# Kernel tuning notes

Measured on AMD Instinct MI355X. Metric: run time of the kernel, lower is better.

## Reference

```python
import jax, jax.numpy as jnp
import numpy as np

P = 16        # patch size
SIM = 0.3     # similarity threshold (forward default arg `sim`)
STY_STD = 1000.0


def patchify(imgs):
    # (N,3,H,W) -> (N, h*w, p*p*3)
    N, C, H, W = imgs.shape
    h, w = H // P, W // P
    x = imgs.reshape(N, C, h, P, w, P)
    x = jnp.einsum('nchpwq->nhwpqc', x)
    return x.reshape(N, h * w, P * P * C)


def setup_inputs() -> dict:
    key = jax.random.key(0)
    k1, k2, k3, k4 = jax.random.split(key, 4)
    N, L, D = 2, 196, 768
    x = jax.random.normal(k1, (N, L + 1, D), dtype=jnp.float32)
    imgs = jax.random.normal(k2, (N, 3, 224, 224), dtype=jnp.float32)
    # torch trunc_normal_(std=1000, a=-2, b=2) == truncated normal on [-2,2]
    learnable_sty = (jax.random.truncated_normal(
        k3, -2.0 / STY_STD, 2.0 / STY_STD, (N, L, L, 1), dtype=jnp.float32) * STY_STD)
    noise = jax.random.normal(k4, (N, L, L, 1), dtype=jnp.float32)
    return {"x": x, "imgs": imgs, "learnable_sty": learnable_sty, "noise": noise}


def reference(x, imgs, learnable_sty, noise):
    imgs = patchify(imgs)                                   # (N, L, 768)
    cls_tokens, x = x[:, :1], x[:, 1:]
    N, L, D = x.shape

    # per-patch normalization (torch.var default is unbiased -> ddof=1)
    mean = imgs.mean(axis=-1, keepdims=True)
    var = jnp.var(imgs, axis=-1, keepdims=True, ddof=1)
    imgs_n = (imgs - mean) / jnp.sqrt(var + 1e-6)
    nrm = jnp.linalg.norm(imgs_n, axis=-1)                  # (N, L)
    Sim = jnp.einsum('aik,ajk->aij', imgs_n, imgs_n) / (nrm[:, :, None] * nrm[:, None, :])

    M0 = jnp.triu((Sim > SIM).astype(jnp.float32))          # (N, L, L), binary
    rows = jnp.arange(L)

    def body(i, M):
        # original loop breaks when sum == N*L; we freeze M once that holds
        done = M.sum() == N * L
        mask = (M[:, i, :] == 0).astype(M.dtype)            # (N, L)
        # rows <= i unchanged (M*M == M for binary), rows > i masked
        upd = jnp.where(rows[None, :, None] > i, M * mask[:, None, :], M)
        return jnp.where(done, M, upd)

    M = jax.lax.fori_loop(0, L - 1, body, M0)

    # decompose: phase (con) keeps grad, amplitude (sty) is detached
    fft = jnp.fft.fftn(x, axes=(-1,))
    con, sty = jnp.angle(fft), jnp.abs(fft)
    sty_d = jax.lax.stop_gradient(sty)

    avg_sum = (M[..., None] * sty_d[:, None, :, :]).sum(axis=2)   # (N, L, D)
    sty_mask = (avg_sum > 0).astype(jnp.float32)                   # (N, L, D)
    num = M.sum(axis=2)[..., None]                                 # (N, L, 1)
    avg = avg_sum / jnp.clip(num, 1e-7, None)                      # (N, L, D)
    std = jnp.sqrt(
        (M[..., None] * (sty_d[:, None, :, :] - avg[:, :, None, :]) ** 2).sum(axis=2)
        / jnp.clip(num, 1e-7, None))                               # (N, L, D)

    sty_para = sty_mask[:, None, :, :] * learnable_sty             # (N, L, L, D)
    sty_para = sty_para / jnp.clip(sty_para.sum(axis=2, keepdims=True), 1e-7, None)
    various = noise * std[:, None, :, :] + avg[:, None, :, :]      # (N, L, L, D)
    sum_sty = (sty_para * various).sum(axis=2)                     # (N, L, D)

    # compose: ifft(amp * e^{i phase}), torch .float() keeps the real part
    out = jnp.real(jnp.fft.ifftn(sum_sty * jnp.exp(1j * con), axes=(-1,))).astype(jnp.float32)
    return jnp.concatenate((cls_tokens, out), axis=1)
```

## Files before the change

kernel.cpp:

```cpp
#include <hip/hip_runtime.h>
#include <math.h>

typedef unsigned long long u64;

#define NBATCH 2
#define LTOK 196
#define DDIM 768
#define NROWS (NBATCH*LTOK)
#define NLD (NBATCH*LTOK*DDIM)

#define PI_F 3.14159265358979323846f
#define S3 0.86602540378443864676f

__device__ __forceinline__ void fft_butterfly(float* re, float* im,
                                              const float2* T,
                                              int tau, int s, int half) {
  int sub = tau >> 7;
  int b = tau & 127;
  int j = b & (half - 1);
  int p0 = (sub << 8) + ((b >> (s - 1)) << s) + j;
  int p1 = p0 + half;
  float2 w = T[j << (8 - s)];
  float xr = re[p1], xi = im[p1];
  float tr = w.x * xr - w.y * xi;
  float ti = w.x * xi + w.y * xr;
  float ur = re[p0], ui = im[p0];
  re[p0] = ur + tr; im[p0] = ui + ti;
  re[p1] = ur - tr; im[p1] = ui - ti;
}

__device__ __forceinline__ void fft_stages(float* re, float* im,
                                           const float2* T, int t) {
#pragma unroll
  for (int s = 1; s <= 8; s++) {
    int half = 1 << (s - 1);
    fft_butterfly(re, im, T, t, s, half);
    if (t < 128) fft_butterfly(re, im, T, t + 256, s, half);
    __syncthreads();
  }
}

__global__ __launch_bounds__(256) void k_pre(const float* __restrict__ imgs,
                                             const float* __restrict__ x,
                                             float* __restrict__ uT,
                                             float* __restrict__ sty,
                                             float* __restrict__ phre,
                                             float* __restrict__ phim) {
  int t = threadIdx.x;
  if (blockIdx.x < NROWS) {
    int blk = blockIdx.x;
    int a = blk / LTOK, l = blk - a * LTOK;
    int hh = l / 14, ww = l - hh * 14;
    float loc[3];
    double s = 0.0, sq = 0.0;
#pragma unroll
    for (int e = 0; e < 3; e++) {
      int d = t + (e << 8);
      int p = d / 48, r = d - p * 48;
      int q2 = r / 3, c = r - q2 * 3;
      float val = imgs[((size_t)(a * 3 + c) * 224 + (hh * 16 + p)) * 224 + (ww * 16 + q2)];
      loc[e] = val;
      s += (double)val;
      sq += (double)val * (double)val;
    }
#pragma unroll
    for (int o = 32; o > 0; o >>= 1) { s += __shfl_down(s, o); sq += __shfl_down(sq, o); }
    __shared__ double rs[4], rq[4];
    __shared__ float sh_mu, sh_sc;
    if ((t & 63) == 0) { rs[t >> 6] = s; rq[t >> 6] = sq; }
    __syncthreads();
    if (t == 0) {
      double S = rs[0] + rs[1] + rs[2] + rs[3];
      double Q = rq[0] + rq[1] + rq[2] + rq[3];
      double mean = S / 768.0;
      double ss = Q - S * S / 768.0;
      if (ss < 1e-30) ss = 1e-30;
      sh_mu = (float)mean;
      sh_sc = (float)(1.0 / sqrt(ss));
    }
    __syncthreads();
    float mu = sh_mu, sc = sh_sc;
    int col = a * LTOK + l;
#pragma unroll
    for (int e = 0; e < 3; e++) {
      int d = t + (e << 8);
      uT[(size_t)d * NROWS + col] = (loc[e] - mu) * sc;
    }
  } else {
    int blk = blockIdx.x - NROWS;
    int a = blk / LTOK, i = blk - a * LTOK;
    __shared__ float re[768], im[768];
    __shared__ float2 t256[128];
    if (t < 128) {
      float sn, cs;
      __sincosf(-2.0f * PI_F * (float)t / 256.0f, &sn, &cs);
      t256[t] = make_float2(cs, sn);
    }
    size_t row = ((size_t)a * (LTOK + 1) + 1 + i) * DDIM;
#pragma unroll
    for (int e = 0; e < 3; e++) {
      int d = t + (e << 8);
      int m = d / 3, r = d - 3 * m;
      int p = (r << 8) + (__brev((unsigned)m) >> 24);
      re[p] = x[row + d];
      im[p] = 0.f;
    }
    __syncthreads();
    fft_stages(re, im, t256, t);
    float a0r = re[t],       a0i = im[t];
    float a1r = re[256 + t], a1i = im[256 + t];
    float a2r = re[512 + t], a2i = im[512 + t];
    float sn, cs;
    __sincosf(-2.0f * PI_F * (float)t / 768.0f, &sn, &cs);
    float2 w1 = make_float2(cs, sn);
    float2 w2 = make_float2(cs * cs - sn * sn, 2.f * cs * sn);
    float b1r = a1r * w1.x - a1i * w1.y, b1i = a1r * w1.y + a1i * w1.x;
    float b2r = a2r * w2.x - a2i * w2.y, b2i = a2r * w2.y + a2i * w2.x;
    float Xr[3], Xi[3];
    Xr[0] = a0r + b1r + b2r;
    Xi[0] = a0i + b1i + b2i;
    Xr[1] = a0r + (-0.5f * b1r + S3 * b1i) + (-0.5f * b2r - S3 * b2i);
    Xi[1] = a0i + (-0.5f * b1i - S3 * b1r) + (-0.5f * b2i + S3 * b2r);
    Xr[2] = a0r + (-0.5f * b1r - S3 * b1i) + (-0.5f * b2r + S3 * b2i);
    Xi[2] = a0i + (-0.5f * b1i + S3 * b1r) + (-0.5f * b2i - S3 * b2r);
    size_t ob = ((size_t)a * LTOK + i) * DDIM + t;
#pragma unroll
    for (int s = 0; s < 3; s++) {
      float mag = sqrtf(Xr[s] * Xr[s] + Xi[s] * Xi[s]);
      size_t o = ob + (s << 8);
      sty[o] = mag;
      if (mag > 0.f) { phre[o] = Xr[s] / mag; phim[o] = Xi[s] / mag; }
      else           { phre[o] = 1.f;         phim[o] = 0.f;         }
    }
  }
}

__global__ __launch_bounds__(256) void k_sim(const float* __restrict__ uT,
                                             u64* __restrict__ Mb) {
  int blk = blockIdx.x;
  int a = blk / LTOK, i = blk - a * LTOK;
  __shared__ float ui[768];
  __shared__ u64 mask[4];
  int t = threadIdx.x;
  if (t < 4) mask[t] = 0ull;
  int coli = a * LTOK + i;
#pragma unroll
  for (int e = 0; e < 3; e++) {
    int d = t + (e << 8);
    ui[d] = uT[(size_t)d * NROWS + coli];
  }
  __syncthreads();
  int j = i + t;
  if (j < LTOK) {
    const float* col = uT + (a * LTOK + j);
    float dot = 0.f;
#pragma unroll 8
    for (int d = 0; d < 768; d++) dot += ui[d] * col[(size_t)d * NROWS];
    if (dot > 0.3f) atomicOr(&mask[j >> 6], 1ull << (j & 63));
  }
  __syncthreads();
  if (t < 4) Mb[((size_t)a * LTOK + i) * 4 + t] = mask[t];
}

__global__ __launch_bounds__(256) void k_greedy(u64* __restrict__ Mb) {
  __shared__ u64 Ml[NROWS * 4];
  __shared__ int red[4];
  __shared__ int Sdone;
  int t = threadIdx.x;
  for (int w = t; w < NROWS * 4; w += 256) Ml[w] = Mb[w];
  __syncthreads();
  for (int i = 0; i < LTOK - 1; i++) {
    int s = 0;
    for (int w = t; w < NROWS * 4; w += 256) s += __popcll(Ml[w]);
#pragma unroll
    for (int o = 32; o > 0; o >>= 1) s += __shfl_down(s, o);
    if ((t & 63) == 0) red[t >> 6] = s;
    __syncthreads();
    if (t == 0) Sdone = ((red[0] + red[1] + red[2] + red[3]) == NROWS) ? 1 : 0;
    __syncthreads();
    if (Sdone) break;
    for (int w = t; w < NROWS * 4; w += 256) {
      int a = w / (LTOK * 4);
      int rem = w - a * (LTOK * 4);
      int r = rem >> 2, wi = rem & 3;
      if (r > i) Ml[w] &= ~Ml[(a * LTOK + i) * 4 + wi];
    }
    __syncthreads();
  }
  for (int w = t; w < NROWS * 4; w += 256) Mb[w] = Ml[w];
}

__global__ __launch_bounds__(256) void k_stats(const u64* __restrict__ Mb,
                                               const float* __restrict__ sty,
                                               float* __restrict__ savg,
                                               float* __restrict__ sstd,
                                               float* __restrict__ smsk) {
  int blk = blockIdx.x;
  int a = blk / LTOK, i = blk - a * LTOK;
  __shared__ u64 mrow[4];
  int t = threadIdx.x;
  if (t < 4) mrow[t] = Mb[((size_t)a * LTOK + i) * 4 + t];
  __syncthreads();
  int num = __popcll(mrow[0]) + __popcll(mrow[1]) + __popcll(mrow[2]) + __popcll(mrow[3]);
  float fnum = fmaxf((float)num, 1e-7f);
  float acc0 = 0.f, acc1 = 0.f, acc2 = 0.f;
  for (int w = 0; w < 4; w++) {
    u64 m = mrow[w];
    while (m) {
      int b = __ffsll(m) - 1; m &= (m - 1);
      int j = (w << 6) + b;
      const float* sr = sty + ((size_t)a * LTOK + j) * DDIM;
      acc0 += sr[t]; acc1 += sr[t + 256]; acc2 += sr[t + 512];
    }
  }
  float av0 = acc0 / fnum, av1 = acc1 / fnum, av2 = acc2 / fnum;
  float sq0 = 0.f, sq1 = 0.f, sq2 = 0.f;
  for (int w = 0; w < 4; w++) {
    u64 m = mrow[w];
    while (m) {
      int b = __ffsll(m) - 1; m &= (m - 1);
      int j = (w << 6) + b;
      const float* sr = sty + ((size_t)a * LTOK + j) * DDIM;
      float d0 = sr[t] - av0, d1 = sr[t + 256] - av1, d2 = sr[t + 512] - av2;
      sq0 += d0 * d0; sq1 += d1 * d1; sq2 += d2 * d2;
    }
  }
  size_t o = ((size_t)a * LTOK + i) * DDIM + t;
  float mk0 = acc0 > 0.f ? 1.f : 0.f;
  float mk1 = acc1 > 0.f ? 1.f : 0.f;
  float mk2 = acc2 > 0.f ? 1.f : 0.f;
  smsk[o] = mk0;            smsk[o + 256] = mk1;            smsk[o + 512] = mk2;
  savg[o] = mk0 * av0;      savg[o + 256] = mk1 * av1;      savg[o + 512] = mk2 * av2;
  sstd[o] = mk0 * sqrtf(sq0 / fnum);
  sstd[o + 256] = mk1 * sqrtf(sq1 / fnum);
  sstd[o + 512] = mk2 * sqrtf(sq2 / fnum);
}

#define RTILE 7
#define JCH 4
#define JLEN 49
__global__ __launch_bounds__(256) void k_combine_part(const float* __restrict__ ls,
                                                      const float* __restrict__ nz,
                                                      const float* __restrict__ savg,
                                                      const float* __restrict__ sstd,
                                                      const float* __restrict__ smsk,
                                                      float* __restrict__ numP,
                                                      float* __restrict__ denP) {
  int blk = blockIdx.x;
  int a = blk / 336;
  int rem = blk - a * 336;
  int it = rem / 12;
  int r2 = rem - it * 12;
  int dc = r2 >> 2;
  int jc = r2 & 3;
  int i0 = it * RTILE;
  int j0 = jc * JLEN;
  int t = threadIdx.x;
  int d = (dc << 8) + t;
  __shared__ float lsr[RTILE][JLEN], lnr[RTILE][JLEN];
  for (int idx = t; idx < RTILE * JLEN; idx += 256) {
    int ii = idx / JLEN, j = idx - ii * JLEN;
    size_t o = ((size_t)(a * LTOK + i0 + ii)) * LTOK + j0 + j;
    float l = ls[o];
    lsr[ii][j] = l;
    lnr[ii][j] = l * nz[o];
  }
  __syncthreads();
  float nm[RTILE], dn[RTILE];
#pragma unroll
  for (int ii = 0; ii < RTILE; ii++) { nm[ii] = 0.f; dn[ii] = 0.f; }
#pragma unroll 7
  for (int j = 0; j < JLEN; j++) {
    size_t b = ((size_t)(a * LTOK + j0 + j)) * DDIM + d;
    float sd = sstd[b], sv = savg[b], sm = smsk[b];
#pragma unroll
    for (int ii = 0; ii < RTILE; ii++) {
      nm[ii] += lnr[ii][j] * sd;
      nm[ii] += lsr[ii][j] * sv;
      dn[ii] += lsr[ii][j] * sm;
    }
  }
#pragma unroll
  for (int ii = 0; ii < RTILE; ii++) {
    size_t o = ((size_t)jc * NROWS + (a * LTOK + i0 + ii)) * DDIM + d;
    numP[o] = nm[ii];
    denP[o] = dn[ii];
  }
}

__global__ __launch_bounds__(256) void k_ifft(const float* __restrict__ x,
                                              const float* __restrict__ numP,
                                              const float* __restrict__ denP,
                                              const float* __restrict__ phre,
                                              const float* __restrict__ phim,
                                              float* __restrict__ out) {
  int blk = blockIdx.x;
  int t = threadIdx.x;
  if (blk < NBATCH) {
    size_t b = (size_t)blk * (LTOK + 1) * DDIM;
    out[b + t] = x[b + t];
    out[b + t + 256] = x[b + t + 256];
    out[b + t + 512] = x[b + t + 512];
    return;
  }
  int rr = blk - NBATCH;
  int a = rr / LTOK, i = rr - a * LTOK;
  __shared__ float re[768], im[768];
  __shared__ float2 t256[128];
  if (t < 128) {
    float sn, cs;
    __sincosf(2.0f * PI_F * (float)t / 256.0f, &sn, &cs);
    t256[t] = make_float2(cs, sn);
  }
  size_t rowz = ((size_t)a * LTOK + i) * DDIM;
#pragma unroll
  for (int e = 0; e < 3; e++) {
    int d = t + (e << 8);
    float num = 0.f, den = 0.f;
#pragma unroll
    for (int jc = 0; jc < JCH; jc++) {
      size_t o = (size_t)jc * NROWS * DDIM + rowz + d;
      num += numP[o];
      den += denP[o];
    }
    float mg = num / fmaxf(den, 1e-7f);
    int m = d / 3, r = d - 3 * m;
    int p = (r << 8) + (__brev((unsigned)m) >> 24);
    re[p] = mg * phre[rowz + d];
    im[p] = mg * phim[rowz + d];
  }
  __syncthreads();
  fft_stages(re, im, t256, t);
  float a0r = re[t],       a0i = im[t];
  float a1r = re[256 + t], a1i = im[256 + t];
  float a2r = re[512 + t], a2i = im[512 + t];
  float sn, cs;
  __sincosf(2.0f * PI_F * (float)t / 768.0f, &sn, &cs);
  float2 w1 = make_float2(cs, sn);
  float2 w2 = make_float2(cs * cs - sn * sn, 2.f * cs * sn);
  float b1r = a1r * w1.x - a1i * w1.y, b1i = a1r * w1.y + a1i * w1.x;
  float b2r = a2r * w2.x - a2i * w2.y, b2i = a2r * w2.y + a2i * w2.x;
  float Xr[3];
  Xr[0] = a0r + b1r + b2r;
  Xr[1] = a0r + (-0.5f * b1r - S3 * b1i) + (-0.5f * b2r + S3 * b2i);
  Xr[2] = a0r + (-0.5f * b1r + S3 * b1i) + (-0.5f * b2r - S3 * b2i);
  size_t ob = ((size_t)a * (LTOK + 1) + 1 + i) * DDIM + t;
  const float inv = 1.0f / 768.0f;
  out[ob]       = Xr[0] * inv;
  out[ob + 256] = Xr[1] * inv;
  out[ob + 512] = Xr[2] * inv;
}

extern "C" void kernel_launch(void* const* d_in, const int* in_sizes, int n_in,
                              void* d_out, int out_size, void* d_ws, size_t ws_size,
                              hipStream_t stream) {
  (void)in_sizes; (void)n_in; (void)out_size; (void)ws_size;
  const float* x    = (const float*)d_in[0];
  const float* imgs = (const float*)d_in[1];
  const float* ls   = (const float*)d_in[2];
  const float* nz   = (const float*)d_in[3];
  float* out = (float*)d_out;

  float* wf   = (float*)d_ws;
  float* uT   = wf;
  float* sty  = wf + (size_t)NLD;
  float* phre = wf + 2 * (size_t)NLD;
  float* phim = wf + 3 * (size_t)NLD;
  float* sstd = wf + 4 * (size_t)NLD;
  float* smsk = wf + 5 * (size_t)NLD;
  float* numP = wf + 6 * (size_t)NLD;
  float* denP = wf + 10 * (size_t)NLD;
  u64* Mb = (u64*)(wf + 14 * (size_t)NLD);

  k_pre         <<<2 * NROWS, 256, 0, stream>>>(imgs, x, uT, sty, phre, phim);
  k_sim         <<<NROWS, 256, 0, stream>>>(uT, Mb);
  k_greedy      <<<1, 256, 0, stream>>>(Mb);
  k_stats       <<<NROWS, 256, 0, stream>>>(Mb, sty, uT , sstd, smsk);
  k_combine_part<<<NBATCH * 28 * 3 * JCH, 256, 0, stream>>>(ls, nz, uT , sstd, smsk, numP, denP);
  k_ifft        <<<NBATCH + NROWS, 256, 0, stream>>>(x, numP, denP, phre, phim, out);
}
```

Measured before the change: 125.4 us.

## Fuse sim, FFT and greedy into one kernel; recompute stats inside combine

Restructures the pipeline from six launches to four. The FFT now runs alongside the similarity blocks, and a last-block-done atomic counter runs the greedy suppression pass inside that same kernel, so the separate single-block launch goes away. Per-row avg/std/mask are no longer stored; the combine kernel recomputes them from the mask bits and sty for each j. This drops the stats kernel and its intermediate buffers but repeats the gather work once per i-tile (28x) and relies on cross-block memory fences for correctness.

```diff
diff --git a/kernel.cpp b/kernel.cpp
--- a/kernel.cpp
+++ b/kernel.cpp
@@ -11,6 +11,10 @@
 
 #define PI_F 3.14159265358979323846f
 #define S3 0.86602540378443864676f
+
+#define RT 7
+#define JCH 4
+#define JLEN 49
 
 __device__ __forceinline__ void fft_butterfly(float* re, float* im,
                                               const float2* T,
@@ -40,61 +44,75 @@
   }
 }
 
-__global__ __launch_bounds__(256) void k_pre(const float* __restrict__ imgs,
-                                             const float* __restrict__ x,
-                                             float* __restrict__ uT,
-                                             float* __restrict__ sty,
-                                             float* __restrict__ phre,
-                                             float* __restrict__ phim) {
+__global__ __launch_bounds__(256) void k_patch(const float* __restrict__ imgs,
+                                               float* __restrict__ uT,
+                                               unsigned int* __restrict__ counter) {
+  int blk = blockIdx.x;
+  int a = blk / LTOK, l = blk - a * LTOK;
+  int hh = l / 14, ww = l - hh * 14;
   int t = threadIdx.x;
-  if (blockIdx.x < NROWS) {
-    int blk = blockIdx.x;
-    int a = blk / LTOK, l = blk - a * LTOK;
-    int hh = l / 14, ww = l - hh * 14;
-    float loc[3];
-    double s = 0.0, sq = 0.0;
-#pragma unroll
-    for (int e = 0; e < 3; e++) {
-      int d = t + (e << 8);
-      int p = d / 48, r = d - p * 48;
-      int q2 = r / 3, c = r - q2 * 3;
-      float val = imgs[((size_t)(a * 3 + c) * 224 + (hh * 16 + p)) * 224 + (ww * 16 + q2)];
-      loc[e] = val;
-      s += (double)val;
-      sq += (double)val * (double)val;
-    }
-#pragma unroll
-    for (int o = 32; o > 0; o >>= 1) { s += __shfl_down(s, o); sq += __shfl_down(sq, o); }
-    __shared__ double rs[4], rq[4];
-    __shared__ float sh_mu, sh_sc;
-    if ((t & 63) == 0) { rs[t >> 6] = s; rq[t >> 6] = sq; }
-    __syncthreads();
-    if (t == 0) {
-      double S = rs[0] + rs[1] + rs[2] + rs[3];
-      double Q = rq[0] + rq[1] + rq[2] + rq[3];
-      double mean = S / 768.0;
-      double ss = Q - S * S / 768.0;
-      if (ss < 1e-30) ss = 1e-30;
-      sh_mu = (float)mean;
-      sh_sc = (float)(1.0 / sqrt(ss));
-    }
-    __syncthreads();
-    float mu = sh_mu, sc = sh_sc;
-    int col = a * LTOK + l;
-#pragma unroll
-    for (int e = 0; e < 3; e++) {
-      int d = t + (e << 8);
-      uT[(size_t)d * NROWS + col] = (loc[e] - mu) * sc;
-    }
-  } else {
+  if (blk == 0 && t == 0) *counter = 0u;
+  float loc[3];
+  double s = 0.0, sq = 0.0;
+#pragma unroll
+  for (int e = 0; e < 3; e++) {
+    int d = t + (e << 8);
+    int p = d / 48, r = d - p * 48;
+    int q2 = r / 3, c = r - q2 * 3;
+    float val = imgs[((size_t)(a * 3 + c) * 224 + (hh * 16 + p)) * 224 + (ww * 16 + q2)];
+    loc[e] = val;
+    s += (double)val;
+    sq += (double)val * (double)val;
+  }
+#pragma unroll
+  for (int o = 32; o > 0; o >>= 1) { s += __shfl_down(s, o); sq += __shfl_down(sq, o); }
+  __shared__ double rs[4], rq[4];
+  __shared__ float sh_mu, sh_sc;
+  if ((t & 63) == 0) { rs[t >> 6] = s; rq[t >> 6] = sq; }
+  __syncthreads();
+  if (t == 0) {
+    double S = rs[0] + rs[1] + rs[2] + rs[3];
+    double Q = rq[0] + rq[1] + rq[2] + rq[3];
+    double mean = S / 768.0;
+    double ss = Q - S * S / 768.0;
+    if (ss < 1e-30) ss = 1e-30;
+    sh_mu = (float)mean;
+    sh_sc = (float)(1.0 / sqrt(ss));
+  }
+  __syncthreads();
+  float mu = sh_mu, sc = sh_sc;
+  int col = a * LTOK + l;
+#pragma unroll
+  for (int e = 0; e < 3; e++) {
+    int d = t + (e << 8);
+    uT[(size_t)d * NROWS + col] = (loc[e] - mu) * sc;
+  }
+}
+
+union SimSMem {
+  struct { float ui[768]; u64 mask[4]; } sim;
+  struct { u64 Ml[NROWS * 4]; int red[4]; int done; } greedy;
+  struct { float re[768]; float im[768]; float2 t256[128]; } fft;
+};
+
+__global__ __launch_bounds__(256) void k_simfft(const float* __restrict__ uT,
+                                                const float* __restrict__ x,
+                                                float* __restrict__ sty,
+                                                float* __restrict__ phre,
+                                                float* __restrict__ phim,
+                                                u64* __restrict__ Mb,
+                                                unsigned int* __restrict__ counter) {
+  __shared__ SimSMem sm;
+  __shared__ int s_last;
+  int t = threadIdx.x;
+
+  if (blockIdx.x >= NROWS) {
     int blk = blockIdx.x - NROWS;
     int a = blk / LTOK, i = blk - a * LTOK;
-    __shared__ float re[768], im[768];
-    __shared__ float2 t256[128];
     if (t < 128) {
       float sn, cs;
       __sincosf(-2.0f * PI_F * (float)t / 256.0f, &sn, &cs);
-      t256[t] = make_float2(cs, sn);
+      sm.fft.t256[t] = make_float2(cs, sn);
     }
     size_t row = ((size_t)a * (LTOK + 1) + 1 + i) * DDIM;
 #pragma unroll
@@ -102,14 +120,14 @@
       int d = t + (e << 8);
       int m = d / 3, r = d - 3 * m;
       int p = (r << 8) + (__brev((unsigned)m) >> 24);
-      re[p] = x[row + d];
-      im[p] = 0.f;
-    }
-    __syncthreads();
-    fft_stages(re, im, t256, t);
-    float a0r = re[t],       a0i = im[t];
-    float a1r = re[256 + t], a1i = im[256 + t];
-    float a2r = re[512 + t], a2i = im[512 + t];
+      sm.fft.re[p] = x[row + d];
+      sm.fft.im[p] = 0.f;
+    }
+    __syncthreads();
+    fft_stages(sm.fft.re, sm.fft.im, sm.fft.t256, t);
+    float a0r = sm.fft.re[t],       a0i = sm.fft.im[t];
+    float a1r = sm.fft.re[256 + t], a1i = sm.fft.im[256 + t];
+    float a2r = sm.fft.re[512 + t], a2i = sm.fft.im[512 + t];
     float sn, cs;
     __sincosf(-2.0f * PI_F * (float)t / 768.0f, &sn, &cs);
     float2 w1 = make_float2(cs, sn);
@@ -132,120 +150,73 @@
       if (mag > 0.f) { phre[o] = Xr[s] / mag; phim[o] = Xi[s] / mag; }
       else           { phre[o] = 1.f;         phim[o] = 0.f;         }
     }
-  }
-}
-
-__global__ __launch_bounds__(256) void k_sim(const float* __restrict__ uT,
-                                             u64* __restrict__ Mb) {
-  int blk = blockIdx.x;
-  int a = blk / LTOK, i = blk - a * LTOK;
-  __shared__ float ui[768];
-  __shared__ u64 mask[4];
-  int t = threadIdx.x;
-  if (t < 4) mask[t] = 0ull;
-  int coli = a * LTOK + i;
-#pragma unroll
-  for (int e = 0; e < 3; e++) {
-    int d = t + (e << 8);
-    ui[d] = uT[(size_t)d * NROWS + coli];
-  }
-  __syncthreads();
-  int j = i + t;
-  if (j < LTOK) {
-    const float* col = uT + (a * LTOK + j);
-    float dot = 0.f;
+    return;
+  }
+
+  {
+    int task = blockIdx.x;
+    int a = task / LTOK, i = task - a * LTOK;
+    if (t < 4) sm.sim.mask[t] = 0ull;
+    int coli = a * LTOK + i;
+#pragma unroll
+    for (int e = 0; e < 3; e++) {
+      int d = t + (e << 8);
+      sm.sim.ui[d] = uT[(size_t)d * NROWS + coli];
+    }
+    __syncthreads();
+    int j = i + t;
+    if (j < LTOK) {
+      const float* col = uT + (a * LTOK + j);
+      float dot = 0.f;
 #pragma unroll 8
-    for (int d = 0; d < 768; d++) dot += ui[d] * col[(size_t)d * NROWS];
-    if (dot > 0.3f) atomicOr(&mask[j >> 6], 1ull << (j & 63));
-  }
-  __syncthreads();
-  if (t < 4) Mb[((size_t)a * LTOK + i) * 4 + t] = mask[t];
-}
-
-__global__ __launch_bounds__(256) void k_greedy(u64* __restrict__ Mb) {
-  __shared__ u64 Ml[NROWS * 4];
-  __shared__ int red[4];
-  __shared__ int Sdone;
-  int t = threadIdx.x;
-  for (int w = t; w < NROWS * 4; w += 256) Ml[w] = Mb[w];
+      for (int d = 0; d < 768; d++) dot += sm.sim.ui[d] * col[(size_t)d * NROWS];
+      if (dot > 0.3f) atomicOr(&sm.sim.mask[j >> 6], 1ull << (j & 63));
+    }
+    __syncthreads();
+    if (t < 4) Mb[((size_t)a * LTOK + i) * 4 + t] = sm.sim.mask[t];
+  }
+  __syncthreads();
+  if (t == 0) {
+    __threadfence();
+    unsigned prev = atomicAdd(counter, 1u);
+    s_last = (prev == NROWS - 1) ? 1 : 0;
+  }
+  __syncthreads();
+  if (!s_last) return;
+
+  __threadfence();
+  for (int w = t; w < NROWS * 4; w += 256)
+    sm.greedy.Ml[w] = __hip_atomic_load(&Mb[w], __ATOMIC_ACQUIRE, __HIP_MEMORY_SCOPE_AGENT);
   __syncthreads();
   for (int i = 0; i < LTOK - 1; i++) {
     int s = 0;
-    for (int w = t; w < NROWS * 4; w += 256) s += __popcll(Ml[w]);
+    for (int w = t; w < NROWS * 4; w += 256) s += __popcll(sm.greedy.Ml[w]);
 #pragma unroll
     for (int o = 32; o > 0; o >>= 1) s += __shfl_down(s, o);
-    if ((t & 63) == 0) red[t >> 6] = s;
-    __syncthreads();
-    if (t == 0) Sdone = ((red[0] + red[1] + red[2] + red[3]) == NROWS) ? 1 : 0;
-    __syncthreads();
-    if (Sdone) break;
+    if ((t & 63) == 0) sm.greedy.red[t >> 6] = s;
+    __syncthreads();
+    if (t == 0)
+      sm.greedy.done = ((sm.greedy.red[0] + sm.greedy.red[1] +
+                         sm.greedy.red[2] + sm.greedy.red[3]) == NROWS) ? 1 : 0;
+    __syncthreads();
+    if (sm.greedy.done) break;
     for (int w = t; w < NROWS * 4; w += 256) {
       int a = w / (LTOK * 4);
       int rem = w - a * (LTOK * 4);
       int r = rem >> 2, wi = rem & 3;
-      if (r > i) Ml[w] &= ~Ml[(a * LTOK + i) * 4 + wi];
-    }
-    __syncthreads();
-  }
-  for (int w = t; w < NROWS * 4; w += 256) Mb[w] = Ml[w];
-}
-
-__global__ __launch_bounds__(256) void k_stats(const u64* __restrict__ Mb,
-                                               const float* __restrict__ sty,
-                                               float* __restrict__ savg,
-                                               float* __restrict__ sstd,
-                                               float* __restrict__ smsk) {
-  int blk = blockIdx.x;
-  int a = blk / LTOK, i = blk - a * LTOK;
-  __shared__ u64 mrow[4];
-  int t = threadIdx.x;
-  if (t < 4) mrow[t] = Mb[((size_t)a * LTOK + i) * 4 + t];
-  __syncthreads();
-  int num = __popcll(mrow[0]) + __popcll(mrow[1]) + __popcll(mrow[2]) + __popcll(mrow[3]);
-  float fnum = fmaxf((float)num, 1e-7f);
-  float acc0 = 0.f, acc1 = 0.f, acc2 = 0.f;
-  for (int w = 0; w < 4; w++) {
-    u64 m = mrow[w];
-    while (m) {
-      int b = __ffsll(m) - 1; m &= (m - 1);
-      int j = (w << 6) + b;
-      const float* sr = sty + ((size_t)a * LTOK + j) * DDIM;
-      acc0 += sr[t]; acc1 += sr[t + 256]; acc2 += sr[t + 512];
-    }
-  }
-  float av0 = acc0 / fnum, av1 = acc1 / fnum, av2 = acc2 / fnum;
-  float sq0 = 0.f, sq1 = 0.f, sq2 = 0.f;
-  for (int w = 0; w < 4; w++) {
-    u64 m = mrow[w];
-    while (m) {
-      int b = __ffsll(m) - 1; m &= (m - 1);
-      int j = (w << 6) + b;
-      const float* sr = sty + ((size_t)a * LTOK + j) * DDIM;
-      float d0 = sr[t] - av0, d1 = sr[t + 256] - av1, d2 = sr[t + 512] - av2;
-      sq0 += d0 * d0; sq1 += d1 * d1; sq2 += d2 * d2;
-    }
-  }
-  size_t o = ((size_t)a * LTOK + i) * DDIM + t;
-  float mk0 = acc0 > 0.f ? 1.f : 0.f;
-  float mk1 = acc1 > 0.f ? 1.f : 0.f;
-  float mk2 = acc2 > 0.f ? 1.f : 0.f;
-  smsk[o] = mk0;            smsk[o + 256] = mk1;            smsk[o + 512] = mk2;
-  savg[o] = mk0 * av0;      savg[o + 256] = mk1 * av1;      savg[o + 512] = mk2 * av2;
-  sstd[o] = mk0 * sqrtf(sq0 / fnum);
-  sstd[o + 256] = mk1 * sqrtf(sq1 / fnum);
-  sstd[o + 512] = mk2 * sqrtf(sq2 / fnum);
-}
-
-#define RTILE 7
-#define JCH 4
-#define JLEN 49
-__global__ __launch_bounds__(256) void k_combine_part(const float* __restrict__ ls,
-                                                      const float* __restrict__ nz,
-                                                      const float* __restrict__ savg,
-                                                      const float* __restrict__ sstd,
-                                                      const float* __restrict__ smsk,
-                                                      float* __restrict__ numP,
-                                                      float* __restrict__ denP) {
+      if (r > i) sm.greedy.Ml[w] &= ~sm.greedy.Ml[(a * LTOK + i) * 4 + wi];
+    }
+    __syncthreads();
+  }
+  for (int w = t; w < NROWS * 4; w += 256) Mb[w] = sm.greedy.Ml[w];
+}
+
+__global__ __launch_bounds__(256) void k_combstats(const float* __restrict__ ls,
+                                                   const float* __restrict__ nz,
+                                                   const float* __restrict__ sty,
+                                                   const u64* __restrict__ Mb,
+                                                   float* __restrict__ numP,
+                                                   float* __restrict__ denP) {
   int blk = blockIdx.x;
   int a = blk / 336;
   int rem = blk - a * 336;
@@ -253,12 +224,12 @@
   int r2 = rem - it * 12;
   int dc = r2 >> 2;
   int jc = r2 & 3;
-  int i0 = it * RTILE;
+  int i0 = it * RT;
   int j0 = jc * JLEN;
   int t = threadIdx.x;
   int d = (dc << 8) + t;
-  __shared__ float lsr[RTILE][JLEN], lnr[RTILE][JLEN];
-  for (int idx = t; idx < RTILE * JLEN; idx += 256) {
+  __shared__ float lsr[RT][JLEN], lnr[RT][JLEN];
+  for (int idx = t; idx < RT * JLEN; idx += 256) {
     int ii = idx / JLEN, j = idx - ii * JLEN;
     size_t o = ((size_t)(a * LTOK + i0 + ii)) * LTOK + j0 + j;
     float l = ls[o];
@@ -266,22 +237,49 @@
     lnr[ii][j] = l * nz[o];
   }
   __syncthreads();
-  float nm[RTILE], dn[RTILE];
-#pragma unroll
-  for (int ii = 0; ii < RTILE; ii++) { nm[ii] = 0.f; dn[ii] = 0.f; }
-#pragma unroll 7
+  float nm[RT], dn[RT];
+#pragma unroll
+  for (int ii = 0; ii < RT; ii++) { nm[ii] = 0.f; dn[ii] = 0.f; }
   for (int j = 0; j < JLEN; j++) {
-    size_t b = ((size_t)(a * LTOK + j0 + j)) * DDIM + d;
-    float sd = sstd[b], sv = savg[b], sm = smsk[b];
-#pragma unroll
-    for (int ii = 0; ii < RTILE; ii++) {
-      nm[ii] += lnr[ii][j] * sd;
-      nm[ii] += lsr[ii][j] * sv;
-      dn[ii] += lsr[ii][j] * sm;
-    }
-  }
-#pragma unroll
-  for (int ii = 0; ii < RTILE; ii++) {
+    int jj = j0 + j;
+    const u64* mp = Mb + ((size_t)a * LTOK + jj) * 4;
+    u64 mr[4] = {mp[0], mp[1], mp[2], mp[3]};
+    int num = __popcll(mr[0]) + __popcll(mr[1]) + __popcll(mr[2]) + __popcll(mr[3]);
+    float fnum = fmaxf((float)num, 1e-7f);
+    float acc = 0.f;
+#pragma unroll
+    for (int w = 0; w < 4; w++) {
+      u64 m = mr[w];
+      while (m) {
+        int b = __ffsll(m) - 1; m &= (m - 1);
+        int k = (w << 6) + b;
+        acc += sty[((size_t)a * LTOK + k) * DDIM + d];
+      }
+    }
+    float av = acc / fnum;
+    float sq = 0.f;
+#pragma unroll
+    for (int w = 0; w < 4; w++) {
+      u64 m = mr[w];
+      while (m) {
+        int b = __ffsll(m) - 1; m &= (m - 1);
+        int k = (w << 6) + b;
+        float dv = sty[((size_t)a * LTOK + k) * DDIM + d] - av;
+        sq += dv * dv;
+      }
+    }
+    float smv = acc > 0.f ? 1.f : 0.f;
+    float msd = smv * sqrtf(sq / fnum);
+    float mav = smv * av;
+#pragma unroll
+    for (int ii = 0; ii < RT; ii++) {
+      nm[ii] += lnr[ii][j] * msd;
+      nm[ii] += lsr[ii][j] * mav;
+      dn[ii] += lsr[ii][j] * smv;
+    }
+  }
+#pragma unroll
+  for (int ii = 0; ii < RT; ii++) {
     size_t o = ((size_t)jc * NROWS + (a * LTOK + i0 + ii)) * DDIM + d;
     numP[o] = nm[ii];
     denP[o] = dn[ii];
@@ -366,16 +364,13 @@
   float* sty  = wf + (size_t)NLD;
   float* phre = wf + 2 * (size_t)NLD;
   float* phim = wf + 3 * (size_t)NLD;
-  float* sstd = wf + 4 * (size_t)NLD;
-  float* smsk = wf + 5 * (size_t)NLD;
-  float* numP = wf + 6 * (size_t)NLD;
-  float* denP = wf + 10 * (size_t)NLD;
-  u64* Mb = (u64*)(wf + 14 * (size_t)NLD);
-
-  k_pre         <<<2 * NROWS, 256, 0, stream>>>(imgs, x, uT, sty, phre, phim);
-  k_sim         <<<NROWS, 256, 0, stream>>>(uT, Mb);
-  k_greedy      <<<1, 256, 0, stream>>>(Mb);
-  k_stats       <<<NROWS, 256, 0, stream>>>(Mb, sty, uT , sstd, smsk);
-  k_combine_part<<<NBATCH * 28 * 3 * JCH, 256, 0, stream>>>(ls, nz, uT , sstd, smsk, numP, denP);
-  k_ifft        <<<NBATCH + NROWS, 256, 0, stream>>>(x, numP, denP, phre, phim, out);
-}
+  float* numP = wf + 4 * (size_t)NLD;
+  float* denP = wf + 8 * (size_t)NLD;
+  u64* Mb = (u64*)(wf + 12 * (size_t)NLD);
+  unsigned int* counter = (unsigned int*)(Mb + NROWS * 4);
+
+  k_patch    <<<NROWS, 256, 0, stream>>>(imgs, uT, counter);
+  k_simfft   <<<2 * NROWS, 256, 0, stream>>>(uT, x, sty, phre, phim, Mb, counter);
+  k_combstats<<<NBATCH * 28 * 3 * JCH, 256, 0, stream>>>(ls, nz, sty, Mb, numP, denP);
+  k_ifft     <<<NBATCH + NROWS, 256, 0, stream>>>(x, numP, denP, phre, phim, out);
+}
```

After: 149.5 us. +19.2%, slower.

## Fuse greedy pass into similarity kernel via last-block counter, coalesce patch loads

Applied to the files above, without the earlier changes.

Folds the single-block greedy suppression kernel into the similarity kernel: the last block to finish, detected with a global atomic counter, runs the greedy loop, which removes one kernel launch. The cls-token copy moves from the ifft kernel into extra blocks of the pre kernel, and those blocks also reset the counter. Patch pixel loads now use a (p,q) thread mapping so reads along image rows are contiguous. A row-major copy of the normalized patches is written so the similarity kernel loads its own row coalesced, at the cost of an extra buffer write. The greedy step still runs on a single block, now as the tail of the similarity kernel.

```diff
diff --git a/kernel.cpp b/kernel.cpp
--- a/kernel.cpp
+++ b/kernel.cpp
@@ -11,6 +11,10 @@
 
 #define PI_F 3.14159265358979323846f
 #define S3 0.86602540378443864676f
+
+#define RT 7
+#define JCH 4
+#define JLEN 49
 
 __device__ __forceinline__ void fft_butterfly(float* re, float* im,
                                               const float2* T,
@@ -42,24 +46,34 @@
 
 __global__ __launch_bounds__(256) void k_pre(const float* __restrict__ imgs,
                                              const float* __restrict__ x,
+                                             float* __restrict__ u,
                                              float* __restrict__ uT,
                                              float* __restrict__ sty,
                                              float* __restrict__ phre,
-                                             float* __restrict__ phim) {
+                                             float* __restrict__ phim,
+                                             float* __restrict__ out,
+                                             unsigned int* __restrict__ counter) {
   int t = threadIdx.x;
+  if (blockIdx.x >= 2 * NROWS) {
+    int a = blockIdx.x - 2 * NROWS;
+    if (a == 0 && t == 0) *counter = 0u;
+    size_t b = (size_t)a * (LTOK + 1) * DDIM;
+    out[b + t] = x[b + t];
+    out[b + t + 256] = x[b + t + 256];
+    out[b + t + 512] = x[b + t + 512];
+    return;
+  }
   if (blockIdx.x < NROWS) {
     int blk = blockIdx.x;
     int a = blk / LTOK, l = blk - a * LTOK;
     int hh = l / 14, ww = l - hh * 14;
+    int p = t >> 4, q = t & 15;
     float loc[3];
     double s = 0.0, sq = 0.0;
 #pragma unroll
-    for (int e = 0; e < 3; e++) {
-      int d = t + (e << 8);
-      int p = d / 48, r = d - p * 48;
-      int q2 = r / 3, c = r - q2 * 3;
-      float val = imgs[((size_t)(a * 3 + c) * 224 + (hh * 16 + p)) * 224 + (ww * 16 + q2)];
-      loc[e] = val;
+    for (int c = 0; c < 3; c++) {
+      float val = imgs[((size_t)(a * 3 + c) * 224 + (hh * 16 + p)) * 224 + (ww * 16 + q)];
+      loc[c] = val;
       s += (double)val;
       sq += (double)val * (double)val;
     }
@@ -81,10 +95,13 @@
     __syncthreads();
     float mu = sh_mu, sc = sh_sc;
     int col = a * LTOK + l;
-#pragma unroll
-    for (int e = 0; e < 3; e++) {
-      int d = t + (e << 8);
-      uT[(size_t)d * NROWS + col] = (loc[e] - mu) * sc;
+    size_t rbase = (size_t)col * DDIM;
+#pragma unroll
+    for (int c = 0; c < 3; c++) {
+      int d = 3 * t + c;
+      float v = (loc[c] - mu) * sc;
+      u[rbase + d] = v;
+      uT[(size_t)d * NROWS + col] = v;
     }
   } else {
     int blk = blockIdx.x - NROWS;
@@ -135,59 +152,74 @@
   }
 }
 
-__global__ __launch_bounds__(256) void k_sim(const float* __restrict__ uT,
-                                             u64* __restrict__ Mb) {
-  int blk = blockIdx.x;
-  int a = blk / LTOK, i = blk - a * LTOK;
-  __shared__ float ui[768];
-  __shared__ u64 mask[4];
+union SimSMem {
+  struct { float ui[768]; u64 mask[4]; } sim;
+  struct { u64 Ml[NROWS * 4]; int red[4]; int done; } greedy;
+};
+
+__global__ __launch_bounds__(256) void k_sim(const float* __restrict__ u,
+                                             const float* __restrict__ uT,
+                                             u64* __restrict__ Mb,
+                                             unsigned int* __restrict__ counter) {
+  __shared__ SimSMem sm;
+  __shared__ int s_last;
   int t = threadIdx.x;
-  if (t < 4) mask[t] = 0ull;
-  int coli = a * LTOK + i;
-#pragma unroll
-  for (int e = 0; e < 3; e++) {
-    int d = t + (e << 8);
-    ui[d] = uT[(size_t)d * NROWS + coli];
-  }
-  __syncthreads();
-  int j = i + t;
-  if (j < LTOK) {
-    const float* col = uT + (a * LTOK + j);
-    float dot = 0.f;
+  {
+    int task = blockIdx.x;
+    int a = task / LTOK, i = task - a * LTOK;
+    if (t < 4) sm.sim.mask[t] = 0ull;
+    size_t rbase = ((size_t)a * LTOK + i) * DDIM;
+#pragma unroll
+    for (int e = 0; e < 3; e++) {
+      int d = t + (e << 8);
+      sm.sim.ui[d] = u[rbase + d];
+    }
+    __syncthreads();
+    int j = i + t;
+    if (j < LTOK) {
+      const float* col = uT + (a * LTOK + j);
+      float dot = 0.f;
 #pragma unroll 8
-    for (int d = 0; d < 768; d++) dot += ui[d] * col[(size_t)d * NROWS];
-    if (dot > 0.3f) atomicOr(&mask[j >> 6], 1ull << (j & 63));
-  }
-  __syncthreads();
-  if (t < 4) Mb[((size_t)a * LTOK + i) * 4 + t] = mask[t];
-}
-
-__global__ __launch_bounds__(256) void k_greedy(u64* __restrict__ Mb) {
-  __shared__ u64 Ml[NROWS * 4];
-  __shared__ int red[4];
-  __shared__ int Sdone;
-  int t = threadIdx.x;
-  for (int w = t; w < NROWS * 4; w += 256) Ml[w] = Mb[w];
+      for (int d = 0; d < 768; d++) dot += sm.sim.ui[d] * col[(size_t)d * NROWS];
+      if (dot > 0.3f) atomicOr(&sm.sim.mask[j >> 6], 1ull << (j & 63));
+    }
+    __syncthreads();
+    if (t < 4) Mb[((size_t)a * LTOK + i) * 4 + t] = sm.sim.mask[t];
+  }
+  __syncthreads();
+  if (t == 0) {
+    __threadfence();
+    unsigned prev = atomicAdd(counter, 1u);
+    s_last = (prev == NROWS - 1) ? 1 : 0;
+  }
+  __syncthreads();
+  if (!s_last) return;
+
+  __threadfence();
+  for (int w = t; w < NROWS * 4; w += 256)
+    sm.greedy.Ml[w] = __hip_atomic_load(&Mb[w], __ATOMIC_ACQUIRE, __HIP_MEMORY_SCOPE_AGENT);
   __syncthreads();
   for (int i = 0; i < LTOK - 1; i++) {
     int s = 0;
-    for (int w = t; w < NROWS * 4; w += 256) s += __popcll(Ml[w]);
+    for (int w = t; w < NROWS * 4; w += 256) s += __popcll(sm.greedy.Ml[w]);
 #pragma unroll
     for (int o = 32; o > 0; o >>= 1) s += __shfl_down(s, o);
-    if ((t & 63) == 0) red[t >> 6] = s;
-    __syncthreads();
-    if (t == 0) Sdone = ((red[0] + red[1] + red[2] + red[3]) == NROWS) ? 1 : 0;
-    __syncthreads();
-    if (Sdone) break;
+    if ((t & 63) == 0) sm.greedy.red[t >> 6] = s;
+    __syncthreads();
+    if (t == 0)
+      sm.greedy.done = ((sm.greedy.red[0] + sm.greedy.red[1] +
+                         sm.greedy.red[2] + sm.greedy.red[3]) == NROWS) ? 1 : 0;
+    __syncthreads();
+    if (sm.greedy.done) break;
     for (int w = t; w < NROWS * 4; w += 256) {
       int a = w / (LTOK * 4);
       int rem = w - a * (LTOK * 4);
       int r = rem >> 2, wi = rem & 3;
-      if (r > i) Ml[w] &= ~Ml[(a * LTOK + i) * 4 + wi];
-    }
-    __syncthreads();
-  }
-  for (int w = t; w < NROWS * 4; w += 256) Mb[w] = Ml[w];
+      if (r > i) sm.greedy.Ml[w] &= ~sm.greedy.Ml[(a * LTOK + i) * 4 + wi];
+    }
+    __syncthreads();
+  }
+  for (int w = t; w < NROWS * 4; w += 256) Mb[w] = sm.greedy.Ml[w];
 }
 
 __global__ __launch_bounds__(256) void k_stats(const u64* __restrict__ Mb,
@@ -236,16 +268,13 @@
   sstd[o + 512] = mk2 * sqrtf(sq2 / fnum);
 }
 
-#define RTILE 7
-#define JCH 4
-#define JLEN 49
-__global__ __launch_bounds__(256) void k_combine_part(const float* __restrict__ ls,
-                                                      const float* __restrict__ nz,
-                                                      const float* __restrict__ savg,
-                                                      const float* __restrict__ sstd,
-                                                      const float* __restrict__ smsk,
-                                                      float* __restrict__ numP,
-                                                      float* __restrict__ denP) {
+__global__ __launch_bounds__(256) void k_comb(const float* __restrict__ ls,
+                                              const float* __restrict__ nz,
+                                              const float* __restrict__ savg,
+                                              const float* __restrict__ sstd,
+                                              const float* __restrict__ smsk,
+                                              float* __restrict__ numP,
+                                              float* __restrict__ denP) {
   int blk = blockIdx.x;
   int a = blk / 336;
   int rem = blk - a * 336;
@@ -253,12 +282,12 @@
   int r2 = rem - it * 12;
   int dc = r2 >> 2;
   int jc = r2 & 3;
-  int i0 = it * RTILE;
+  int i0 = it * RT;
   int j0 = jc * JLEN;
   int t = threadIdx.x;
   int d = (dc << 8) + t;
-  __shared__ float lsr[RTILE][JLEN], lnr[RTILE][JLEN];
-  for (int idx = t; idx < RTILE * JLEN; idx += 256) {
+  __shared__ float lsr[RT][JLEN], lnr[RT][JLEN];
+  for (int idx = t; idx < RT * JLEN; idx += 256) {
     int ii = idx / JLEN, j = idx - ii * JLEN;
     size_t o = ((size_t)(a * LTOK + i0 + ii)) * LTOK + j0 + j;
     float l = ls[o];
@@ -266,44 +295,35 @@
     lnr[ii][j] = l * nz[o];
   }
   __syncthreads();
-  float nm[RTILE], dn[RTILE];
-#pragma unroll
-  for (int ii = 0; ii < RTILE; ii++) { nm[ii] = 0.f; dn[ii] = 0.f; }
+  float nm[RT], dn[RT];
+#pragma unroll
+  for (int ii = 0; ii < RT; ii++) { nm[ii] = 0.f; dn[ii] = 0.f; }
 #pragma unroll 7
   for (int j = 0; j < JLEN; j++) {
     size_t b = ((size_t)(a * LTOK + j0 + j)) * DDIM + d;
     float sd = sstd[b], sv = savg[b], sm = smsk[b];
 #pragma unroll
-    for (int ii = 0; ii < RTILE; ii++) {
+    for (int ii = 0; ii < RT; ii++) {
       nm[ii] += lnr[ii][j] * sd;
       nm[ii] += lsr[ii][j] * sv;
       dn[ii] += lsr[ii][j] * sm;
     }
   }
 #pragma unroll
-  for (int ii = 0; ii < RTILE; ii++) {
+  for (int ii = 0; ii < RT; ii++) {
     size_t o = ((size_t)jc * NROWS + (a * LTOK + i0 + ii)) * DDIM + d;
     numP[o] = nm[ii];
     denP[o] = dn[ii];
   }
 }
 
-__global__ __launch_bounds__(256) void k_ifft(const float* __restrict__ x,
-                                              const float* __restrict__ numP,
+__global__ __launch_bounds__(256) void k_ifft(const float* __restrict__ numP,
                                               const float* __restrict__ denP,
                                               const float* __restrict__ phre,
                                               const float* __restrict__ phim,
                                               float* __restrict__ out) {
-  int blk = blockIdx.x;
+  int rr = blockIdx.x;
   int t = threadIdx.x;
-  if (blk < NBATCH) {
-    size_t b = (size_t)blk * (LTOK + 1) * DDIM;
-    out[b + t] = x[b + t];
-    out[b + t + 256] = x[b + t + 256];
-    out[b + t + 512] = x[b + t + 512];
-    return;
-  }
-  int rr = blk - NBATCH;
   int a = rr / LTOK, i = rr - a * LTOK;
   __shared__ float re[768], im[768];
   __shared__ float2 t256[128];
@@ -362,20 +382,22 @@
   float* out = (float*)d_out;
 
   float* wf   = (float*)d_ws;
-  float* uT   = wf;
-  float* sty  = wf + (size_t)NLD;
-  float* phre = wf + 2 * (size_t)NLD;
-  float* phim = wf + 3 * (size_t)NLD;
-  float* sstd = wf + 4 * (size_t)NLD;
-  float* smsk = wf + 5 * (size_t)NLD;
-  float* numP = wf + 6 * (size_t)NLD;
-  float* denP = wf + 10 * (size_t)NLD;
-  u64* Mb = (u64*)(wf + 14 * (size_t)NLD);
-
-  k_pre         <<<2 * NROWS, 256, 0, stream>>>(imgs, x, uT, sty, phre, phim);
-  k_sim         <<<NROWS, 256, 0, stream>>>(uT, Mb);
-  k_greedy      <<<1, 256, 0, stream>>>(Mb);
-  k_stats       <<<NROWS, 256, 0, stream>>>(Mb, sty, uT , sstd, smsk);
-  k_combine_part<<<NBATCH * 28 * 3 * JCH, 256, 0, stream>>>(ls, nz, uT , sstd, smsk, numP, denP);
-  k_ifft        <<<NBATCH + NROWS, 256, 0, stream>>>(x, numP, denP, phre, phim, out);
-}
+  float* u    = wf;
+  float* uT   = wf + (size_t)NLD;
+  float* sty  = wf + 2 * (size_t)NLD;
+  float* phre = wf + 3 * (size_t)NLD;
+  float* phim = wf + 4 * (size_t)NLD;
+  float* savg = wf + 5 * (size_t)NLD;
+  float* sstd = wf + 6 * (size_t)NLD;
+  float* smsk = wf + 7 * (size_t)NLD;
+  float* numP = wf + 8 * (size_t)NLD;
+  float* denP = wf + 12 * (size_t)NLD;
+  u64* Mb = (u64*)(wf + 16 * (size_t)NLD);
+  unsigned int* counter = (unsigned int*)(Mb + NROWS * 4);
+
+  k_pre  <<<2 * NROWS + NBATCH, 256, 0, stream>>>(imgs, x, u, uT, sty, phre, phim, out, counter);
+  k_sim  <<<NROWS, 256, 0, stream>>>(u, uT, Mb, counter);
+  k_stats<<<NROWS, 256, 0, stream>>>(Mb, sty, savg, sstd, smsk);
+  k_comb <<<NBATCH * 28 * 3 * JCH, 256, 0, stream>>>(ls, nz, savg, sstd, smsk, numP, denP);
+  k_ifft <<<NROWS, 256, 0, stream>>>(numP, denP, phre, phim, out);
+}
```

Result: slower. 147.8 us (+17.9%).
